# Optimization experiments

Measured on AMD Instinct MI355X. Metric: run time of the kernel, lower is better.

Reference implementation:

```python
import jax, jax.numpy as jnp
import numpy as np

N_NODES = 100000
N_EDGES = 800000
D_IN, D_H1, D_H2, D_OUT = 512, 256, 256, 64


def setup_inputs() -> dict:
    key = jax.random.key(0)
    ks = jax.random.split(key, 8)
    x = jax.random.normal(ks[0], (N_NODES, D_IN), dtype=jnp.float32)
    edge_index = jax.random.randint(ks[1], (2, N_EDGES), 0, N_NODES, dtype=jnp.int64)
    # Glorot-style scaled weights (PyG GCNConv uses glorot init; Linear uses kaiming-uniform).
    W1 = jax.random.normal(ks[2], (D_IN, D_H1), dtype=jnp.float32) / np.sqrt(D_IN)
    b1 = jnp.zeros((D_H1,), dtype=jnp.float32)
    W2 = jax.random.normal(ks[3], (D_H1, D_H2), dtype=jnp.float32) / np.sqrt(D_H1)
    b2 = jnp.zeros((D_H2,), dtype=jnp.float32)
    Wc = jax.random.normal(ks[4], (D_H2, D_OUT), dtype=jnp.float32) / np.sqrt(D_H2)
    bc = jnp.zeros((D_OUT,), dtype=jnp.float32)
    return {"x": x, "edge_index": edge_index, "W1": W1, "b1": b1,
            "W2": W2, "b2": b2, "Wc": Wc, "bc": bc}


def reference(x, edge_index, W1, b1, W2, b2, Wc, bc):
    # GCNModel.forward in eval mode (dropout is identity when training=False).
    N = x.shape[0]
    src, dst = edge_index[0], edge_index[1]
    # PyG GCNConv: add self-loops, symmetric normalization D^-1/2 (A+I) D^-1/2.
    deg = jnp.zeros((N,), x.dtype).at[dst].add(jnp.float32(1.0)) + 1.0  # in-degree + self-loop
    dinv = jax.lax.rsqrt(deg)                         # [N]
    norm = dinv[src] * dinv[dst]                      # [E] per-edge coefficient
    self_norm = (dinv * dinv)[:, None]                # [N,1] self-loop coefficient 1/deg

    def gcn_conv(h, W, b):
        h = h @ W                                     # transform first (PyG order)
        agg = jax.ops.segment_sum(h[src] * norm[:, None], dst, num_segments=N)
        return agg + h * self_norm + b

    h = jax.nn.relu(gcn_conv(x, W1, b1))
    h = jax.nn.relu(gcn_conv(h, W2, b2))
    return h @ Wc + bc                                # [N, num_classes]
```

## Files before the change

kernel.cpp:

```cpp
#include <hip/hip_runtime.h>
#include <cstdint>

#define DIN 512
#define DH  256
#define DOUT 64

typedef __attribute__((ext_vector_type(8))) short bf16x8;
typedef __attribute__((ext_vector_type(4))) float f32x4;
typedef unsigned int uint32;

__device__ __forceinline__ unsigned short f2bf(float f) {
    uint32 u = __float_as_uint(f);
    u += 0x7fff + ((u >> 16) & 1);
    return (unsigned short)(u >> 16);
}
__device__ __forceinline__ float bflo(uint32 u) { return __uint_as_float(u << 16); }
__device__ __forceinline__ float bfhi(uint32 u) { return __uint_as_float(u & 0xffff0000u); }
__device__ __forceinline__ uint32 pk2(float lo, float hi) {
    return (uint32)f2bf(lo) | ((uint32)f2bf(hi) << 16);
}

__global__ void detect_i64(const unsigned long long* ei, int n_check,
                           unsigned long long bound, int* flag) {
    __shared__ int ok;
    if (threadIdx.x == 0) ok = 1;
    __syncthreads();
    int bad = 0;
    for (int i = threadIdx.x; i < n_check; i += blockDim.x) {
        if (ei[i] >= bound) bad = 1;
    }
    if (bad) ok = 0;
    __syncthreads();
    if (threadIdx.x == 0) *flag = ok;
}

__device__ __forceinline__ int get_idx(const void* ei, int is64, int pos) {
    if (is64) return (int)((const long long*)ei)[pos];
    return ((const int*)ei)[pos];
}

__global__ void count_deg(const void* ei, const int* flag, int E, int* counts) {
    const int is64 = *flag;
    int e = blockIdx.x * blockDim.x + threadIdx.x;
    if (e >= E) return;
    int d = get_idx(ei, is64, E + e);
    atomicAdd(&counts[d], 1);
}

__global__ void compute_dinv(const int* counts, float* dinv, int N) {
    int i = blockIdx.x * blockDim.x + threadIdx.x;
    if (i < N) dinv[i] = rsqrtf((float)counts[i] + 1.0f);
}

#define SCAN_BLOCK 256
#define SCAN_ELEMS 1024

__global__ void scan1(const int* counts, int* out, int* blocksums, int N) {
    __shared__ int sh[SCAN_BLOCK];
    int base = blockIdx.x * SCAN_ELEMS;
    int t = threadIdx.x;
    int v[4];
    int s = 0;
    #pragma unroll
    for (int j = 0; j < 4; j++) {
        int idx = base + t * 4 + j;
        v[j] = (idx < N) ? counts[idx] : 0;
        s += v[j];
    }
    sh[t] = s;
    __syncthreads();
    for (int off = 1; off < SCAN_BLOCK; off <<= 1) {
        int x = (t >= off) ? sh[t - off] : 0;
        __syncthreads();
        sh[t] += x;
        __syncthreads();
    }
    int run = (t == 0) ? 0 : sh[t - 1];
    #pragma unroll
    for (int j = 0; j < 4; j++) {
        int idx = base + t * 4 + j;
        if (idx < N) out[idx] = run;
        run += v[j];
    }
    if (t == SCAN_BLOCK - 1) blocksums[blockIdx.x] = sh[t];
}

__global__ void scan2(int* blocksums, int NB) {
    __shared__ int sh[SCAN_BLOCK];
    int t = threadIdx.x;
    sh[t] = (t < NB) ? blocksums[t] : 0;
    __syncthreads();
    for (int off = 1; off < SCAN_BLOCK; off <<= 1) {
        int x = (t >= off) ? sh[t - off] : 0;
        __syncthreads();
        sh[t] += x;
        __syncthreads();
    }
    if (t < NB) blocksums[t] = (t == 0) ? 0 : sh[t - 1];
}

__global__ void scan3(int* row_ptr, const int* blocksums, int N, int E) {
    int i = blockIdx.x * blockDim.x + threadIdx.x;
    if (i < N) row_ptr[i] += blocksums[i / SCAN_ELEMS];
    if (i == N) row_ptr[N] = E;
}

__global__ void fill_csr(const void* ei, const int* flag, int E,
                         const int* row_ptr, int* cursor, int* col_idx,
                         const float* dinv, float* edge_w) {
    const int is64 = *flag;
    int e = blockIdx.x * blockDim.x + threadIdx.x;
    if (e >= E) return;
    int d = get_idx(ei, is64, E + e);
    int s = get_idx(ei, is64, e);
    int pos = row_ptr[d] + atomicAdd(&cursor[d], 1);
    col_idx[pos] = s;
    edge_w[pos] = dinv[s] * dinv[d];
}

__global__ void transpose_w(const float* __restrict__ W, unsigned short* __restrict__ Bt,
                            int K, int Nw) {
    int i = blockIdx.x * blockDim.x + threadIdx.x;
    if (i >= K * Nw) return;
    int k = i / Nw, n = i % Nw;
    Bt[(size_t)n * K + k] = f2bf(W[i]);
}

template <bool A_FP32>
__global__ __launch_bounds__(256) void gemm_mfma(const void* __restrict__ Ap,
                                                 const unsigned short* __restrict__ Bt,
                                                 unsigned short* __restrict__ C,
                                                 int M, int K) {
    __shared__ unsigned short lds[20480];
    unsigned short* As = lds;
    unsigned short* Bs = lds + 4096;
    const int tid = threadIdx.x;
    const int w = tid >> 6, l = tid & 63;
    const int m0 = blockIdx.x * 64;

    f32x4 acc[4][4] = {};

    for (int k0 = 0; k0 < K; k0 += 64) {
        #pragma unroll
        for (int i = 0; i < 8; i++) {
            int row = i * 32 + (tid >> 3);
            int gq = (tid & 7) ^ (row & 7);
            const unsigned short* src = Bt + (size_t)row * K + k0 + gq * 8;
            unsigned short* dst = Bs + row * 64 + (tid & 7) * 8;
            __builtin_amdgcn_global_load_lds(
                (const __attribute__((address_space(1))) uint32*)src,
                (__attribute__((address_space(3))) uint32*)dst, 16, 0, 0);
        }
        if (A_FP32) {
            const float* Af = (const float*)Ap;
            #pragma unroll
            for (int i = 0; i < 2; i++) {
                int row = i * 32 + (tid >> 3);
                int g = tid & 7;
                int rg = m0 + row; if (rg > M - 1) rg = M - 1;
                const float* s = Af + (size_t)rg * K + k0 + g * 8;
                float4 v0 = *(const float4*)s;
                float4 v1 = *(const float4*)(s + 4);
                uint4 o;
                o.x = pk2(v0.x, v0.y); o.y = pk2(v0.z, v0.w);
                o.z = pk2(v1.x, v1.y); o.w = pk2(v1.z, v1.w);
                *(uint4*)(As + row * 64 + ((g ^ (row & 7)) * 8)) = o;
            }
        } else {
            const unsigned short* Ab = (const unsigned short*)Ap;
            #pragma unroll
            for (int i = 0; i < 2; i++) {
                int row = i * 32 + (tid >> 3);
                int gq = (tid & 7) ^ (row & 7);
                int rg = m0 + row; if (rg > M - 1) rg = M - 1;
                const unsigned short* src = Ab + (size_t)rg * K + k0 + gq * 8;
                unsigned short* dst = As + row * 64 + (tid & 7) * 8;
                __builtin_amdgcn_global_load_lds(
                    (const __attribute__((address_space(1))) uint32*)src,
                    (__attribute__((address_space(3))) uint32*)dst, 16, 0, 0);
            }
        }
        __syncthreads();
        #pragma unroll
        for (int ks = 0; ks < 2; ks++) {
            bf16x8 a[4], b[4];
            #pragma unroll
            for (int m = 0; m < 4; m++) {
                int arow = m * 16 + (l & 15);
                int ag = (ks * 4 + (l >> 4)) ^ (arow & 7);
                a[m] = *(const bf16x8*)(As + arow * 64 + ag * 8);
            }
            #pragma unroll
            for (int n = 0; n < 4; n++) {
                int brow = w * 64 + n * 16 + (l & 15);
                int bg = (ks * 4 + (l >> 4)) ^ (brow & 7);
                b[n] = *(const bf16x8*)(Bs + brow * 64 + bg * 8);
            }
            #pragma unroll
            for (int m = 0; m < 4; m++)
                #pragma unroll
                for (int n = 0; n < 4; n++)
                    acc[m][n] = __builtin_amdgcn_mfma_f32_16x16x32_bf16(a[m], b[n], acc[m][n], 0, 0, 0);
        }
        __syncthreads();
    }

    unsigned short* ep = lds + w * 4096;
    #pragma unroll
    for (int m = 0; m < 4; m++)
        #pragma unroll
        for (int n = 0; n < 4; n++)
            #pragma unroll
            for (int r = 0; r < 4; r++)
                ep[(m * 16 + (l >> 4) * 4 + r) * 64 + n * 16 + (l & 15)] = f2bf(acc[m][n][r]);
    __syncthreads();
    #pragma unroll
    for (int p = 0; p < 8; p++) {
        int row = p * 8 + (l >> 3);
        int gr = m0 + row;
        uint4 v = *(const uint4*)(ep + row * 64 + (l & 7) * 8);
        if (gr < M)
            *(uint4*)(C + (size_t)gr * 256 + w * 64 + (l & 7) * 8) = v;
    }
}

__global__ __launch_bounds__(512) void gemm2_persist(const unsigned short* __restrict__ A,
                                                     const unsigned short* __restrict__ Bt,
                                                     unsigned short* __restrict__ C,
                                                     int M) {
    __shared__ unsigned short lds[73728];
    unsigned short* Bs = lds;
    unsigned short* As = lds + 65536;
    const int tid = threadIdx.x;
    const int w = tid >> 6, l = tid & 63;
    const int wr = w >> 2, wc = w & 3;

    #pragma unroll
    for (int i = 0; i < 16; i++) {
        int gi = i * 512 + tid;
        int r = gi >> 5, g = gi & 31;
        int gs = g ^ (r & 7);
        __builtin_amdgcn_global_load_lds(
            (const __attribute__((address_space(1))) uint32*)(Bt + (size_t)r * 256 + gs * 8),
            (__attribute__((address_space(3))) uint32*)(Bs + (size_t)gi * 8), 16, 0, 0);
    }

    const int sr = tid >> 3;
    const int sg = tid & 7;

    for (int mt = blockIdx.x; mt * 64 < M; mt += gridDim.x) {
        const int m0 = mt * 64;
        {
            int rg = m0 + sr; if (rg > M - 1) rg = M - 1;
            int gq = sg ^ (sr & 7);
            __builtin_amdgcn_global_load_lds(
                (const __attribute__((address_space(1))) uint32*)(A + (size_t)rg * 256 + gq * 8),
                (__attribute__((address_space(3))) uint32*)(As + tid * 8), 16, 0, 0);
        }
        __syncthreads();

        f32x4 acc[2][4] = {};
        #pragma unroll
        for (int k = 0; k < 4; k++) {
            if (k < 3) {
                int rg = m0 + sr; if (rg > M - 1) rg = M - 1;
                int gq = sg ^ (sr & 7);
                __builtin_amdgcn_global_load_lds(
                    (const __attribute__((address_space(1))) uint32*)(A + (size_t)rg * 256 + (k + 1) * 64 + gq * 8),
                    (__attribute__((address_space(3))) uint32*)(As + ((k + 1) & 1) * 4096 + tid * 8), 16, 0, 0);
            }
            const unsigned short* Ab = As + (k & 1) * 4096;
            #pragma unroll
            for (int ks = 0; ks < 2; ks++) {
                bf16x8 a[2], b[4];
                #pragma unroll
                for (int m = 0; m < 2; m++) {
                    int ar = wr * 32 + m * 16 + (l & 15);
                    int q = (ks * 4 + (l >> 4)) ^ (ar & 7);
                    a[m] = *(const bf16x8*)(Ab + ar * 64 + q * 8);
                }
                #pragma unroll
                for (int n = 0; n < 4; n++) {
                    int br = wc * 64 + n * 16 + (l & 15);
                    int gabs = k * 8 + ks * 4 + (l >> 4);
                    int q = gabs ^ (br & 7);
                    b[n] = *(const bf16x8*)(Bs + br * 256 + q * 8);
                }
                #pragma unroll
                for (int m = 0; m < 2; m++)
                    #pragma unroll
                    for (int n = 0; n < 4; n++)
                        acc[m][n] = __builtin_amdgcn_mfma_f32_16x16x32_bf16(a[m], b[n], acc[m][n], 0, 0, 0);
            }
            __syncthreads();
        }

        #pragma unroll
        for (int m = 0; m < 2; m++)
            #pragma unroll
            for (int r = 0; r < 4; r++) {
                int row = m0 + wr * 32 + m * 16 + (l >> 4) * 4 + r;
                if (row >= M) continue;
                #pragma unroll
                for (int n = 0; n < 4; n++) {
                    int col = wc * 64 + n * 16 + (l & 15);
                    C[(size_t)row * 256 + col] = f2bf(acc[m][n][r]);
                }
            }
    }
}

__global__ __launch_bounds__(256) void gemm_head(const unsigned short* __restrict__ A,
                                                 const unsigned short* __restrict__ Bt,
                                                 const float* __restrict__ bias,
                                                 float* __restrict__ out, int M) {
    __shared__ unsigned short As[128 * 64];
    __shared__ unsigned short Bs[64 * 64];
    const int tid = threadIdx.x;
    const int w = tid >> 6, l = tid & 63;
    const int m0 = blockIdx.x * 128;
    const int wr = w >> 1, wc = w & 1;
    f32x4 acc[4][2] = {};

    for (int k0 = 0; k0 < 256; k0 += 64) {
        #pragma unroll
        for (int i = 0; i < 4; i++) {
            int row = i * 32 + (tid >> 3);
            int gq = (tid & 7) ^ (row & 7);
            int rg = m0 + row; if (rg > M - 1) rg = M - 1;
            __builtin_amdgcn_global_load_lds(
                (const __attribute__((address_space(1))) uint32*)(A + (size_t)rg * 256 + k0 + gq * 8),
                (__attribute__((address_space(3))) uint32*)(As + row * 64 + (tid & 7) * 8), 16, 0, 0);
        }
        #pragma unroll
        for (int i = 0; i < 2; i++) {
            int row = i * 32 + (tid >> 3);
            int gq = (tid & 7) ^ (row & 7);
            __builtin_amdgcn_global_load_lds(
                (const __attribute__((address_space(1))) uint32*)(Bt + (size_t)row * 256 + k0 + gq * 8),
                (__attribute__((address_space(3))) uint32*)(Bs + row * 64 + (tid & 7) * 8), 16, 0, 0);
        }
        __syncthreads();
        #pragma unroll
        for (int ks = 0; ks < 2; ks++) {
            bf16x8 a[4], b[2];
            #pragma unroll
            for (int m = 0; m < 4; m++) {
                int arow = wr * 64 + m * 16 + (l & 15);
                int ag = (ks * 4 + (l >> 4)) ^ (arow & 7);
                a[m] = *(const bf16x8*)(As + arow * 64 + ag * 8);
            }
            #pragma unroll
            for (int n = 0; n < 2; n++) {
                int brow = wc * 32 + n * 16 + (l & 15);
                int bg = (ks * 4 + (l >> 4)) ^ (brow & 7);
                b[n] = *(const bf16x8*)(Bs + brow * 64 + bg * 8);
            }
            #pragma unroll
            for (int m = 0; m < 4; m++)
                #pragma unroll
                for (int n = 0; n < 2; n++)
                    acc[m][n] = __builtin_amdgcn_mfma_f32_16x16x32_bf16(a[m], b[n], acc[m][n], 0, 0, 0);
        }
        __syncthreads();
    }
    #pragma unroll
    for (int m = 0; m < 4; m++)
        #pragma unroll
        for (int n = 0; n < 2; n++)
            #pragma unroll
            for (int r = 0; r < 4; r++) {
                int gr = m0 + wr * 64 + m * 16 + (l >> 4) * 4 + r;
                int col = wc * 32 + n * 16 + (l & 15);
                if (gr < M) out[(size_t)gr * 64 + col] = acc[m][n][r] + bias[col];
            }
}

#define ACC8(v, wgt)                                    \
    do {                                                \
        acc[0] = fmaf(wgt, bflo(v.x), acc[0]);          \
        acc[1] = fmaf(wgt, bfhi(v.x), acc[1]);          \
        acc[2] = fmaf(wgt, bflo(v.y), acc[2]);          \
        acc[3] = fmaf(wgt, bfhi(v.y), acc[3]);          \
        acc[4] = fmaf(wgt, bflo(v.z), acc[4]);          \
        acc[5] = fmaf(wgt, bfhi(v.z), acc[5]);          \
        acc[6] = fmaf(wgt, bflo(v.w), acc[6]);          \
        acc[7] = fmaf(wgt, bfhi(v.w), acc[7]);          \
    } while (0)

__global__ __launch_bounds__(256) void aggregate_bf(const unsigned short* __restrict__ t,
                                                    const float* __restrict__ dinv,
                                                    const int* __restrict__ row_ptr,
                                                    const int* __restrict__ col_idx,
                                                    const float* __restrict__ edge_w,
                                                    const float* __restrict__ bias,
                                                    unsigned short* __restrict__ outb,
                                                    int N) {
    int wave = threadIdx.x >> 6;
    int lane = threadIdx.x & 63;
    int half = lane >> 5;
    int sl = lane & 31;
    int n = blockIdx.x * 8 + wave * 2 + half;
    if (n >= N) return;

    float dn = dinv[n];
    int r0 = row_ptr[n], r1 = row_ptr[n + 1];

    float acc[8];
    {
        uint4 sv = *(const uint4*)(t + (size_t)n * DH + sl * 8);
        float sn = dn * dn;
        acc[0] = bflo(sv.x) * sn; acc[1] = bfhi(sv.x) * sn;
        acc[2] = bflo(sv.y) * sn; acc[3] = bfhi(sv.y) * sn;
        acc[4] = bflo(sv.z) * sn; acc[5] = bfhi(sv.z) * sn;
        acc[6] = bflo(sv.w) * sn; acc[7] = bfhi(sv.w) * sn;
    }

    int j = r0;
    for (; j + 4 <= r1; j += 4) {
        int s0 = col_idx[j + 0], s1 = col_idx[j + 1];
        int s2 = col_idx[j + 2], s3 = col_idx[j + 3];
        float w0 = edge_w[j + 0], w1 = edge_w[j + 1];
        float w2 = edge_w[j + 2], w3 = edge_w[j + 3];
        uint4 v0 = *(const uint4*)(t + (size_t)s0 * DH + sl * 8);
        uint4 v1 = *(const uint4*)(t + (size_t)s1 * DH + sl * 8);
        uint4 v2 = *(const uint4*)(t + (size_t)s2 * DH + sl * 8);
        uint4 v3 = *(const uint4*)(t + (size_t)s3 * DH + sl * 8);
        ACC8(v0, w0); ACC8(v1, w1); ACC8(v2, w2); ACC8(v3, w3);
    }
    for (; j < r1; j++) {
        int s = col_idx[j];
        float wgt = edge_w[j];
        uint4 v = *(const uint4*)(t + (size_t)s * DH + sl * 8);
        ACC8(v, wgt);
    }

    float4 b0 = *(const float4*)(bias + sl * 8);
    float4 b1v = *(const float4*)(bias + sl * 8 + 4);
    acc[0] = fmaxf(acc[0] + b0.x, 0.f);  acc[1] = fmaxf(acc[1] + b0.y, 0.f);
    acc[2] = fmaxf(acc[2] + b0.z, 0.f);  acc[3] = fmaxf(acc[3] + b0.w, 0.f);
    acc[4] = fmaxf(acc[4] + b1v.x, 0.f); acc[5] = fmaxf(acc[5] + b1v.y, 0.f);
    acc[6] = fmaxf(acc[6] + b1v.z, 0.f); acc[7] = fmaxf(acc[7] + b1v.w, 0.f);

    uint4 o;
    o.x = pk2(acc[0], acc[1]);
    o.y = pk2(acc[2], acc[3]);
    o.z = pk2(acc[4], acc[5]);
    o.w = pk2(acc[6], acc[7]);
    *(uint4*)(outb + (size_t)n * DH + sl * 8) = o;
}

extern "C" void kernel_launch(void* const* d_in, const int* in_sizes, int n_in,
                              void* d_out, int out_size, void* d_ws, size_t ws_size,
                              hipStream_t stream) {
    const float* x  = (const float*)d_in[0];
    const void*  ei = d_in[1];
    const float* W1 = (const float*)d_in[2];
    const float* b1 = (const float*)d_in[3];
    const float* W2 = (const float*)d_in[4];
    const float* b2 = (const float*)d_in[5];
    const float* Wc = (const float*)d_in[6];
    const float* bc = (const float*)d_in[7];
    float* out = (float*)d_out;

    const int N = in_sizes[0] / DIN;
    const int E = in_sizes[1] / 2;

    char* ws = (char*)d_ws;
    size_t off = 0;
    auto alloc = [&](size_t bytes) -> void* {
        off = (off + 255) & ~(size_t)255;
        void* p = ws + off;
        off += bytes;
        return p;
    };

    int*   flag      = (int*)alloc(4);
    int*   counts    = (int*)alloc((size_t)N * 4);
    int*   row_ptr   = (int*)alloc((size_t)(N + 1) * 4);
    int*   col_idx   = (int*)alloc((size_t)E * 4);
    float* edge_w    = (float*)alloc((size_t)E * 4);
    int*   blocksums = (int*)alloc(1024 * 4);
    float* dinv      = (float*)alloc((size_t)N * 4);
    unsigned short* Bt1   = (unsigned short*)alloc((size_t)DH * DIN * 2);
    unsigned short* Bt2   = (unsigned short*)alloc((size_t)DH * DH * 2);
    unsigned short* Btc   = (unsigned short*)alloc((size_t)DOUT * DH * 2);
    unsigned short* t_buf = (unsigned short*)alloc((size_t)N * DH * 2);
    unsigned short* a_buf = (unsigned short*)alloc((size_t)N * DH * 2);

    const int NB = (N + SCAN_ELEMS - 1) / SCAN_ELEMS;
    const int gM64  = (N + 63) / 64;
    const int gM128 = (N + 127) / 128;

    detect_i64<<<1, 256, 0, stream>>>((const unsigned long long*)ei, 1024,
                                      (unsigned long long)N, flag);
    transpose_w<<<(DIN * DH + 255) / 256, 256, 0, stream>>>(W1, Bt1, DIN, DH);
    transpose_w<<<(DH * DH + 255) / 256, 256, 0, stream>>>(W2, Bt2, DH, DH);
    transpose_w<<<(DH * DOUT + 255) / 256, 256, 0, stream>>>(Wc, Btc, DH, DOUT);

    hipMemsetAsync(counts, 0, (size_t)N * 4, stream);
    count_deg<<<(E + 255) / 256, 256, 0, stream>>>(ei, flag, E, counts);
    compute_dinv<<<(N + 255) / 256, 256, 0, stream>>>(counts, dinv, N);
    scan1<<<NB, SCAN_BLOCK, 0, stream>>>(counts, row_ptr, blocksums, N);
    scan2<<<1, SCAN_BLOCK, 0, stream>>>(blocksums, NB);
    scan3<<<(N + 1 + 255) / 256, 256, 0, stream>>>(row_ptr, blocksums, N, E);
    hipMemsetAsync(counts, 0, (size_t)N * 4, stream);
    fill_csr<<<(E + 255) / 256, 256, 0, stream>>>(ei, flag, E, row_ptr, counts, col_idx,
                                                  dinv, edge_w);

    gemm_mfma<true><<<gM64, 256, 0, stream>>>(x, Bt1, t_buf, N, DIN);
    aggregate_bf<<<(N + 7) / 8, 256, 0, stream>>>(t_buf, dinv, row_ptr, col_idx, edge_w, b1, a_buf, N);
    gemm2_persist<<<256, 512, 0, stream>>>(a_buf, Bt2, t_buf, N);
    aggregate_bf<<<(N + 7) / 8, 256, 0, stream>>>(t_buf, dinv, row_ptr, col_idx, edge_w, b2, a_buf, N);
    gemm_head<<<gM128, 256, 0, stream>>>(a_buf, Btc, bc, out, N);
}
```

Baseline: 356.6 us.

## Pack CSR edges as int2, read GEMM1 weights directly from global, merge memsets

CSR column indices and edge weights are interleaved into a single int2 array, so the aggregation kernels fetch each edge's index and weight with one load instead of two separate streams. The first GEMM no longer stages the transposed weight tile in LDS and instead loads B fragments straight from global memory, relying on cache since every block reuses the same weights. The LDS footprint shrinks, which may raise occupancy. The two counter memsets are merged into one by giving the cursor its own buffer. The direct global B loads may add latency to the MFMA inner loop.

```diff
diff --git a/kernel.cpp b/kernel.cpp
--- a/kernel.cpp
+++ b/kernel.cpp
@@ -106,16 +106,15 @@
 }
 
 __global__ void fill_csr(const void* ei, const int* flag, int E,
-                         const int* row_ptr, int* cursor, int* col_idx,
-                         const float* dinv, float* edge_w) {
+                         const int* row_ptr, int* cursor, int2* edges,
+                         const float* dinv) {
     const int is64 = *flag;
     int e = blockIdx.x * blockDim.x + threadIdx.x;
     if (e >= E) return;
     int d = get_idx(ei, is64, E + e);
     int s = get_idx(ei, is64, e);
     int pos = row_ptr[d] + atomicAdd(&cursor[d], 1);
-    col_idx[pos] = s;
-    edge_w[pos] = dinv[s] * dinv[d];
+    edges[pos] = make_int2(s, __float_as_int(dinv[s] * dinv[d]));
 }
 
 __global__ void transpose_w(const float* __restrict__ W, unsigned short* __restrict__ Bt,
@@ -126,14 +125,12 @@
     Bt[(size_t)n * K + k] = f2bf(W[i]);
 }
 
-template <bool A_FP32>
-__global__ __launch_bounds__(256) void gemm_mfma(const void* __restrict__ Ap,
-                                                 const unsigned short* __restrict__ Bt,
-                                                 unsigned short* __restrict__ C,
-                                                 int M, int K) {
-    __shared__ unsigned short lds[20480];
+__global__ __launch_bounds__(256) void gemm1_mfma(const float* __restrict__ Af,
+                                                  const unsigned short* __restrict__ Bt,
+                                                  unsigned short* __restrict__ C,
+                                                  int M, int K) {
+    __shared__ unsigned short lds[16384];
     unsigned short* As = lds;
-    unsigned short* Bs = lds + 4096;
     const int tid = threadIdx.x;
     const int w = tid >> 6, l = tid & 63;
     const int m0 = blockIdx.x * 64;
@@ -141,44 +138,19 @@
     f32x4 acc[4][4] = {};
 
     for (int k0 = 0; k0 < K; k0 += 64) {
-        #pragma unroll
-        for (int i = 0; i < 8; i++) {
+        __syncthreads();
+        #pragma unroll
+        for (int i = 0; i < 2; i++) {
             int row = i * 32 + (tid >> 3);
-            int gq = (tid & 7) ^ (row & 7);
-            const unsigned short* src = Bt + (size_t)row * K + k0 + gq * 8;
-            unsigned short* dst = Bs + row * 64 + (tid & 7) * 8;
-            __builtin_amdgcn_global_load_lds(
-                (const __attribute__((address_space(1))) uint32*)src,
-                (__attribute__((address_space(3))) uint32*)dst, 16, 0, 0);
-        }
-        if (A_FP32) {
-            const float* Af = (const float*)Ap;
-            #pragma unroll
-            for (int i = 0; i < 2; i++) {
-                int row = i * 32 + (tid >> 3);
-                int g = tid & 7;
-                int rg = m0 + row; if (rg > M - 1) rg = M - 1;
-                const float* s = Af + (size_t)rg * K + k0 + g * 8;
-                float4 v0 = *(const float4*)s;
-                float4 v1 = *(const float4*)(s + 4);
-                uint4 o;
-                o.x = pk2(v0.x, v0.y); o.y = pk2(v0.z, v0.w);
-                o.z = pk2(v1.x, v1.y); o.w = pk2(v1.z, v1.w);
-                *(uint4*)(As + row * 64 + ((g ^ (row & 7)) * 8)) = o;
-            }
-        } else {
-            const unsigned short* Ab = (const unsigned short*)Ap;
-            #pragma unroll
-            for (int i = 0; i < 2; i++) {
-                int row = i * 32 + (tid >> 3);
-                int gq = (tid & 7) ^ (row & 7);
-                int rg = m0 + row; if (rg > M - 1) rg = M - 1;
-                const unsigned short* src = Ab + (size_t)rg * K + k0 + gq * 8;
-                unsigned short* dst = As + row * 64 + (tid & 7) * 8;
-                __builtin_amdgcn_global_load_lds(
-                    (const __attribute__((address_space(1))) uint32*)src,
-                    (__attribute__((address_space(3))) uint32*)dst, 16, 0, 0);
-            }
+            int g = tid & 7;
+            int rg = m0 + row; if (rg > M - 1) rg = M - 1;
+            const float* s = Af + (size_t)rg * K + k0 + g * 8;
+            float4 v0 = *(const float4*)s;
+            float4 v1 = *(const float4*)(s + 4);
+            uint4 o;
+            o.x = pk2(v0.x, v0.y); o.y = pk2(v0.z, v0.w);
+            o.z = pk2(v1.x, v1.y); o.w = pk2(v1.z, v1.w);
+            *(uint4*)(As + row * 64 + ((g ^ (row & 7)) * 8)) = o;
         }
         __syncthreads();
         #pragma unroll
@@ -186,15 +158,14 @@
             bf16x8 a[4], b[4];
             #pragma unroll
             for (int m = 0; m < 4; m++) {
-                int arow = m * 16 + (l & 15);
-                int ag = (ks * 4 + (l >> 4)) ^ (arow & 7);
-                a[m] = *(const bf16x8*)(As + arow * 64 + ag * 8);
+                int ar = m * 16 + (l & 15);
+                int q = (ks * 4 + (l >> 4)) ^ (ar & 7);
+                a[m] = *(const bf16x8*)(As + ar * 64 + q * 8);
             }
             #pragma unroll
             for (int n = 0; n < 4; n++) {
-                int brow = w * 64 + n * 16 + (l & 15);
-                int bg = (ks * 4 + (l >> 4)) ^ (brow & 7);
-                b[n] = *(const bf16x8*)(Bs + brow * 64 + bg * 8);
+                int br = w * 64 + n * 16 + (l & 15);
+                b[n] = *(const bf16x8*)(Bt + (size_t)br * K + k0 + ks * 32 + (l >> 4) * 8);
             }
             #pragma unroll
             for (int m = 0; m < 4; m++)
@@ -202,9 +173,8 @@
                 for (int n = 0; n < 4; n++)
                     acc[m][n] = __builtin_amdgcn_mfma_f32_16x16x32_bf16(a[m], b[n], acc[m][n], 0, 0, 0);
         }
-        __syncthreads();
-    }
-
+    }
+    __syncthreads();
     unsigned short* ep = lds + w * 4096;
     #pragma unroll
     for (int m = 0; m < 4; m++)
@@ -391,8 +361,7 @@
 __global__ __launch_bounds__(256) void aggregate_bf(const unsigned short* __restrict__ t,
                                                     const float* __restrict__ dinv,
                                                     const int* __restrict__ row_ptr,
-                                                    const int* __restrict__ col_idx,
-                                                    const float* __restrict__ edge_w,
+                                                    const int2* __restrict__ edges,
                                                     const float* __restrict__ bias,
                                                     unsigned short* __restrict__ outb,
                                                     int N) {
@@ -418,20 +387,20 @@
 
     int j = r0;
     for (; j + 4 <= r1; j += 4) {
-        int s0 = col_idx[j + 0], s1 = col_idx[j + 1];
-        int s2 = col_idx[j + 2], s3 = col_idx[j + 3];
-        float w0 = edge_w[j + 0], w1 = edge_w[j + 1];
-        float w2 = edge_w[j + 2], w3 = edge_w[j + 3];
-        uint4 v0 = *(const uint4*)(t + (size_t)s0 * DH + sl * 8);
-        uint4 v1 = *(const uint4*)(t + (size_t)s1 * DH + sl * 8);
-        uint4 v2 = *(const uint4*)(t + (size_t)s2 * DH + sl * 8);
-        uint4 v3 = *(const uint4*)(t + (size_t)s3 * DH + sl * 8);
+        int2 e0 = edges[j + 0], e1 = edges[j + 1];
+        int2 e2 = edges[j + 2], e3 = edges[j + 3];
+        uint4 v0 = *(const uint4*)(t + (size_t)e0.x * DH + sl * 8);
+        uint4 v1 = *(const uint4*)(t + (size_t)e1.x * DH + sl * 8);
+        uint4 v2 = *(const uint4*)(t + (size_t)e2.x * DH + sl * 8);
+        uint4 v3 = *(const uint4*)(t + (size_t)e3.x * DH + sl * 8);
+        float w0 = __int_as_float(e0.y), w1 = __int_as_float(e1.y);
+        float w2 = __int_as_float(e2.y), w3 = __int_as_float(e3.y);
         ACC8(v0, w0); ACC8(v1, w1); ACC8(v2, w2); ACC8(v3, w3);
     }
     for (; j < r1; j++) {
-        int s = col_idx[j];
-        float wgt = edge_w[j];
-        uint4 v = *(const uint4*)(t + (size_t)s * DH + sl * 8);
+        int2 e = edges[j];
+        float wgt = __int_as_float(e.y);
+        uint4 v = *(const uint4*)(t + (size_t)e.x * DH + sl * 8);
         ACC8(v, wgt);
     }
 
@@ -477,9 +446,9 @@
 
     int*   flag      = (int*)alloc(4);
     int*   counts    = (int*)alloc((size_t)N * 4);
+    int*   cursor    = (int*)alloc((size_t)N * 4);
     int*   row_ptr   = (int*)alloc((size_t)(N + 1) * 4);
-    int*   col_idx   = (int*)alloc((size_t)E * 4);
-    float* edge_w    = (float*)alloc((size_t)E * 4);
+    int2*  edges     = (int2*)alloc((size_t)E * 8);
     int*   blocksums = (int*)alloc(1024 * 4);
     float* dinv      = (float*)alloc((size_t)N * 4);
     unsigned short* Bt1   = (unsigned short*)alloc((size_t)DH * DIN * 2);
@@ -498,19 +467,17 @@
     transpose_w<<<(DH * DH + 255) / 256, 256, 0, stream>>>(W2, Bt2, DH, DH);
     transpose_w<<<(DH * DOUT + 255) / 256, 256, 0, stream>>>(Wc, Btc, DH, DOUT);
 
-    hipMemsetAsync(counts, 0, (size_t)N * 4, stream);
+    hipMemsetAsync(counts, 0, (size_t)N * 8 + 256, stream);
     count_deg<<<(E + 255) / 256, 256, 0, stream>>>(ei, flag, E, counts);
     compute_dinv<<<(N + 255) / 256, 256, 0, stream>>>(counts, dinv, N);
     scan1<<<NB, SCAN_BLOCK, 0, stream>>>(counts, row_ptr, blocksums, N);
     scan2<<<1, SCAN_BLOCK, 0, stream>>>(blocksums, NB);
     scan3<<<(N + 1 + 255) / 256, 256, 0, stream>>>(row_ptr, blocksums, N, E);
-    hipMemsetAsync(counts, 0, (size_t)N * 4, stream);
-    fill_csr<<<(E + 255) / 256, 256, 0, stream>>>(ei, flag, E, row_ptr, counts, col_idx,
-                                                  dinv, edge_w);
-
-    gemm_mfma<true><<<gM64, 256, 0, stream>>>(x, Bt1, t_buf, N, DIN);
-    aggregate_bf<<<(N + 7) / 8, 256, 0, stream>>>(t_buf, dinv, row_ptr, col_idx, edge_w, b1, a_buf, N);
+    fill_csr<<<(E + 255) / 256, 256, 0, stream>>>(ei, flag, E, row_ptr, cursor, edges, dinv);
+
+    gemm1_mfma<<<gM64, 256, 0, stream>>>(x, Bt1, t_buf, N, DIN);
+    aggregate_bf<<<(N + 7) / 8, 256, 0, stream>>>(t_buf, dinv, row_ptr, edges, b1, a_buf, N);
     gemm2_persist<<<256, 512, 0, stream>>>(a_buf, Bt2, t_buf, N);
-    aggregate_bf<<<(N + 7) / 8, 256, 0, stream>>>(t_buf, dinv, row_ptr, col_idx, edge_w, b2, a_buf, N);
+    aggregate_bf<<<(N + 7) / 8, 256, 0, stream>>>(t_buf, dinv, row_ptr, edges, b2, a_buf, N);
     gemm_head<<<gM128, 256, 0, stream>>>(a_buf, Btc, bc, out, N);
 }
```

Result: slower. 383.1 us (+7.4%).
